# Optimization experiments

Hardware: AMD Instinct MI355X
Metric: run time of the kernel (lower is better)

## Reference

```python
import jax, jax.numpy as jnp
import numpy as np

TWO_PI = 6.283185307179586


def setup_inputs() -> dict:
    key = jax.random.key(0)
    k1, k2, k3, k4, k5, k6 = jax.random.split(key, 6)
    B, T, D = 2, 8192, 1024
    x = jax.random.normal(k1, (B, T, D), dtype=jnp.float32)
    # nn.Linear weights are [out, in]; init with small scale like torch default
    s = 1.0 / np.sqrt(D)
    Wk = jax.random.uniform(k2, (D, D), jnp.float32, -s, s)
    Wv = jax.random.uniform(k3, (D, D), jnp.float32, -s, s)
    Wo = jax.random.uniform(k4, (D, D), jnp.float32, -s, s)
    # random phasor frequencies in [0, 2*pi)
    freqs = jax.random.uniform(k5, (D,), jnp.float32, 0.0, TWO_PI)
    return {"x": x, "Wk": Wk, "Wv": Wv, "Wo": Wo, "freqs": freqs}


def reference(x, Wk, Wv, Wo, freqs):
    B, T, C = x.shape
    # k projection is computed in the original forward but never used downstream
    k_real = x @ Wk.T  # [B,T,D] (dead value, kept for fidelity)
    v_real = x @ Wv.T  # [B,T,D]
    v = v_real.astype(jnp.complex64)
    # rotors: per-position unit phasors exp(i * t * freqs), shape [T, D]
    t = jnp.arange(T, dtype=jnp.float32)
    rotors = jnp.exp(1j * (t[:, None] * freqs[None, :])).astype(jnp.complex64)
    # bind each value with its rotor and accumulate causally (O(N) memory trace)
    memory_trace = jnp.cumsum(v * rotors[None, :, :], axis=1)  # [B,T,D] complex64
    # retrieve by unbinding with the conjugate rotor; take the real component
    retrieved = jnp.real(memory_trace * jnp.conj(rotors)[None, :, :])  # [B,T,D]
    return retrieved @ Wo.T
```

## Files before the change

### kernel.cpp

```cpp
#include <hip/hip_runtime.h>
#include <hip/hip_bf16.h>


#define B_  2
#define T_  8192
#define D_  1024
#define BT_ 16384
#define CS_ 32
#define NCHUNK_ 256

typedef __attribute__((ext_vector_type(4))) float f32x4;
typedef __attribute__((ext_vector_type(8))) short bf16x8;
typedef __attribute__((ext_vector_type(8))) unsigned short ushort8;

static __device__ inline unsigned short f2bf(float f) {
    union { float f; unsigned int u; } a;
    a.f = f;
    unsigned int u = a.u;
    return (unsigned short)((u + 0x7FFFu + ((u >> 16) & 1u)) >> 16);
}
static __device__ inline float bf2f(unsigned short h) {
    union { unsigned int u; float f; } a;
    a.u = ((unsigned int)h) << 16;
    return a.f;
}

__global__ __launch_bounds__(256) void cast_all(const float* __restrict__ x,
                                                const float* __restrict__ Wv,
                                                const float* __restrict__ Wo,
                                                unsigned short* __restrict__ xb,
                                                unsigned short* __restrict__ wvb,
                                                unsigned short* __restrict__ wob) {
    const int nx = BT_ * D_ / 8;
    const int nw = D_ * D_ / 8;
    int i = blockIdx.x * 256 + threadIdx.x;
    const float4* src;
    unsigned short* dst;
    int j;
    if (i < nx)            { src = (const float4*)x;  dst = xb;  j = i; }
    else if (i < nx + nw)  { src = (const float4*)Wv; dst = wvb; j = i - nx; }
    else                   { src = (const float4*)Wo; dst = wob; j = i - nx - nw; }
    float4 a = src[j * 2];
    float4 b = src[j * 2 + 1];
    ushort8 o;
    o[0] = f2bf(a.x); o[1] = f2bf(a.y); o[2] = f2bf(a.z); o[3] = f2bf(a.w);
    o[4] = f2bf(b.x); o[5] = f2bf(b.y); o[6] = f2bf(b.z); o[7] = f2bf(b.w);
    *(ushort8*)&dst[(size_t)j * 8] = o;
}

template <bool BF16OUT, bool FUSE_SUMS>
__global__ __launch_bounds__(512, 2) void gemm_bt(const short* __restrict__ A,
                                                  const short* __restrict__ Bm,
                                                  void* __restrict__ Cout,
                                                  const float* __restrict__ freqs,
                                                  float* __restrict__ csum,
                                                  int M, int N, int K) {
    __shared__ short lds[65536];
    const int tid = threadIdx.x;
    const int lane = tid & 63;
    const int wave = tid >> 6;
    const int wm = wave >> 2, wn = wave & 3;

    const int nb = N >> 8;
    const int id = blockIdx.x;
    const int xcd = id & 7;
    const int slot = id >> 3;
    const int bn = (slot % nb) * 256;
    const int bm = (xcd * ((M >> 8) >> 3) + slot / nb) * 256;

    const int srow = lane >> 3;
    const int sg = lane & 7;
    const size_t cstep = (size_t)64 * K;
    const short* gA = A + (size_t)(bm + wave * 8 + srow) * K + ((sg ^ srow) * 8);
    const short* gB = Bm + (size_t)(bn + wave * 8 + srow) * K + ((sg ^ srow) * 8);

    auto stage1 = [&](int kt, int g) {
        const int c = g & 3;
        const short* src = ((g & 4) ? gB : gA) + c * cstep + kt * 64;
        short* dst = &lds[(kt & 1) * 32768 + ((g & 4) ? 16384 : 0) + c * 4096 + wave * 512];
        __builtin_amdgcn_global_load_lds(
            (const __attribute__((address_space(1))) void*)src,
            (__attribute__((address_space(3))) void*)dst, 16, 0, 0);
    };

    const int l15 = lane & 15;
    const int c4r = lane >> 4;
    const int swz0 = ((c4r) ^ (lane & 7)) * 8;
    const int swz1 = ((4 + c4r) ^ (lane & 7)) * 8;
    const int abase = (wm * 128 + l15) * 64;
    const int bbase = 16384 + (wn * 64 + l15) * 64;

    f32x4 acc[8][4] = {};

    stage1(0, 0); stage1(0, 1); stage1(0, 2); stage1(0, 3);
    stage1(0, 4); stage1(0, 5); stage1(0, 6); stage1(0, 7);
    stage1(1, 0); stage1(1, 2);
    stage1(1, 4); stage1(1, 5); stage1(1, 6); stage1(1, 7);
    asm volatile("s_waitcnt vmcnt(6)" ::: "memory");
    __builtin_amdgcn_sched_barrier(0);
    __builtin_amdgcn_s_barrier();

    const int NT = K >> 6;
#pragma unroll 1
    for (int t = 0; t < NT; ++t) {
        const int sb = (t & 1) * 32768;
        const bool pf = (t + 2 < NT);
        bf16x8 av[4][2], b01[2][2], b23[2][2];

#pragma unroll
        for (int ii = 0; ii < 4; ++ii) {
            av[ii][0] = *(const bf16x8*)&lds[sb + abase + ii * 1024 + swz0];
            av[ii][1] = *(const bf16x8*)&lds[sb + abase + ii * 1024 + swz1];
        }
#pragma unroll
        for (int j = 0; j < 2; ++j) {
            b01[j][0] = *(const bf16x8*)&lds[sb + bbase + j * 1024 + swz0];
            b01[j][1] = *(const bf16x8*)&lds[sb + bbase + j * 1024 + swz1];
        }
        if (t + 1 < NT) { stage1(t + 1, 1); stage1(t + 1, 3); }
        __builtin_amdgcn_s_barrier();
        asm volatile("s_waitcnt lgkmcnt(0)" ::: "memory");
        __builtin_amdgcn_sched_barrier(0);
        __builtin_amdgcn_s_setprio(1);
#pragma unroll
        for (int ks = 0; ks < 2; ++ks)
#pragma unroll
            for (int ii = 0; ii < 4; ++ii)
#pragma unroll
                for (int j = 0; j < 2; ++j)
                    acc[ii][j] = __builtin_amdgcn_mfma_f32_16x16x32_bf16(
                        av[ii][ks], b01[j][ks], acc[ii][j], 0, 0, 0);
        __builtin_amdgcn_s_setprio(0);
        __builtin_amdgcn_s_barrier();

#pragma unroll
        for (int j = 0; j < 2; ++j) {
            b23[j][0] = *(const bf16x8*)&lds[sb + bbase + (2 + j) * 1024 + swz0];
            b23[j][1] = *(const bf16x8*)&lds[sb + bbase + (2 + j) * 1024 + swz1];
        }
        if (pf) { stage1(t + 2, 0); stage1(t + 2, 2); }
        __builtin_amdgcn_s_barrier();
        asm volatile("s_waitcnt lgkmcnt(0)" ::: "memory");
        __builtin_amdgcn_sched_barrier(0);
        __builtin_amdgcn_s_setprio(1);
#pragma unroll
        for (int ks = 0; ks < 2; ++ks)
#pragma unroll
            for (int ii = 0; ii < 4; ++ii)
#pragma unroll
                for (int j = 0; j < 2; ++j)
                    acc[ii][2 + j] = __builtin_amdgcn_mfma_f32_16x16x32_bf16(
                        av[ii][ks], b23[j][ks], acc[ii][2 + j], 0, 0, 0);
        __builtin_amdgcn_s_setprio(0);
        __builtin_amdgcn_s_barrier();

#pragma unroll
        for (int ii = 0; ii < 4; ++ii) {
            av[ii][0] = *(const bf16x8*)&lds[sb + abase + (4 + ii) * 1024 + swz0];
            av[ii][1] = *(const bf16x8*)&lds[sb + abase + (4 + ii) * 1024 + swz1];
        }
        if (pf) { stage1(t + 2, 4); stage1(t + 2, 5); }
        asm volatile("s_waitcnt vmcnt(12)" ::: "memory");
        __builtin_amdgcn_s_barrier();
        asm volatile("s_waitcnt lgkmcnt(0)" ::: "memory");
        __builtin_amdgcn_sched_barrier(0);
        __builtin_amdgcn_s_setprio(1);
#pragma unroll
        for (int ks = 0; ks < 2; ++ks)
#pragma unroll
            for (int ii = 0; ii < 4; ++ii)
#pragma unroll
                for (int j = 0; j < 2; ++j)
                    acc[4 + ii][2 + j] = __builtin_amdgcn_mfma_f32_16x16x32_bf16(
                        av[ii][ks], b23[j][ks], acc[4 + ii][2 + j], 0, 0, 0);
        __builtin_amdgcn_s_setprio(0);
        __builtin_amdgcn_s_barrier();

        if (pf) { stage1(t + 2, 6); stage1(t + 2, 7); }
        if (pf) asm volatile("s_waitcnt vmcnt(8)" ::: "memory");
        else    asm volatile("s_waitcnt vmcnt(0)" ::: "memory");
        __builtin_amdgcn_sched_barrier(0);
        __builtin_amdgcn_s_barrier();
        __builtin_amdgcn_s_setprio(1);
#pragma unroll
        for (int ks = 0; ks < 2; ++ks)
#pragma unroll
            for (int ii = 0; ii < 4; ++ii)
#pragma unroll
                for (int j = 0; j < 2; ++j)
                    acc[4 + ii][j] = __builtin_amdgcn_mfma_f32_16x16x32_bf16(
                        av[ii][ks], b01[j][ks], acc[4 + ii][j], 0, 0, 0);
        __builtin_amdgcn_s_setprio(0);
        __builtin_amdgcn_s_barrier();
    }

    const int row0 = c4r * 4;
#pragma unroll
    for (int i = 0; i < 8; ++i) {
#pragma unroll
        for (int j = 0; j < 4; ++j) {
            const int col = bn + wn * 64 + j * 16 + (lane & 15);
#pragma unroll
            for (int r = 0; r < 4; ++r) {
                const size_t row = (size_t)bm + wm * 128 + i * 16 + row0 + r;
                if constexpr (BF16OUT)
                    ((unsigned short*)Cout)[row * N + col] = f2bf(acc[i][j][r]);
                else
                    ((float*)Cout)[row * N + col] = acc[i][j][r];
            }
        }
    }

    if constexpr (FUSE_SUMS) {
        const int b = bm >> 13;
        const int trow = bm & 8191;
#pragma unroll
        for (int ig2 = 0; ig2 < 4; ++ig2) {
            const int chunk = (trow >> 5) + wm * 4 + ig2;
            const int t0 = trow + wm * 128 + ig2 * 32 + c4r * 4;
#pragma unroll
            for (int j = 0; j < 4; ++j) {
                const int d = bn + wn * 64 + j * 16 + (lane & 15);
                const float f = freqs[d];
                float ss, cc2;
                sincosf((float)t0 * f, &ss, &cc2);
                float s1, c1;
                sincosf(f, &s1, &c1);
                float c2 = c1 * c1 - s1 * s1, s2 = 2.f * c1 * s1;
                float c4 = c2 * c2 - s2 * s2, s4 = 2.f * c2 * s2;
                float c8 = c4 * c4 - s4 * s4, s8 = 2.f * c4 * s4;
                float c12 = c8 * c4 - s8 * s4, s12 = s8 * c4 + c8 * s4;
                float c13 = c12 * c1 - s12 * s1, s13 = s12 * c1 + c12 * s1;
                float ar = 0.f, ai = 0.f;
                float cr = cc2, sr2 = ss;
#pragma unroll
                for (int f2 = 0; f2 < 2; ++f2) {
                    const int i = ig2 * 2 + f2;
#pragma unroll
                    for (int r = 0; r < 4; ++r) {
                        const float w = acc[i][j][r];
                        ar = fmaf(w, cr, ar); ai = fmaf(w, sr2, ai);
                        const float ec = (r < 3) ? c1 : c13;
                        const float es = (r < 3) ? s1 : s13;
                        const float nc = cr * ec - sr2 * es;
                        const float ns = sr2 * ec + cr * es;
                        cr = nc; sr2 = ns;
                    }
                }
                ar += __shfl_xor(ar, 16); ai += __shfl_xor(ai, 16);
                ar += __shfl_xor(ar, 32); ai += __shfl_xor(ai, 32);
                if (c4r == 0)
                    *(float2*)(csum + (((size_t)b * NCHUNK_ + chunk) * D_ + d) * 2) =
                        make_float2(ar, ai);
            }
        }
    }
}

__global__ __launch_bounds__(512) void scan_pass2(float* __restrict__ csum) {
    const int wid = (blockIdx.x * 512 + threadIdx.x) >> 6;
    const int lane = threadIdx.x & 63;
    const int b = wid / D_;
    const int d = wid % D_;
    float2* cs = (float2*)csum;
    const size_t base = (size_t)b * NCHUNK_ * D_ + d;

    float2 s[4];
#pragma unroll
    for (int k = 0; k < 4; ++k)
        s[k] = cs[base + (size_t)(lane * 4 + k) * D_];
    float lr = s[0].x + s[1].x + s[2].x + s[3].x;
    float li = s[0].y + s[1].y + s[2].y + s[3].y;

    float ir = lr, ii = li;
#pragma unroll
    for (int off = 1; off < 64; off <<= 1) {
        float tr = __shfl_up(ir, off);
        float ti = __shfl_up(ii, off);
        if (lane >= off) { ir += tr; ii += ti; }
    }
    float er = ir - lr, ei = ii - li;
#pragma unroll
    for (int k = 0; k < 4; ++k) {
        const float rr = s[k].x, rim = s[k].y;
        cs[base + (size_t)(lane * 4 + k) * D_] = make_float2(er, ei);
        er += rr; ei += rim;
    }
}

__global__ __launch_bounds__(256) void scan_pass3(const unsigned short* __restrict__ v,
                                                  const float* __restrict__ freqs,
                                                  const float* __restrict__ csum,
                                                  unsigned short* __restrict__ ret) {
    const int chunk = blockIdx.x;
    const int d0 = blockIdx.y * 512 + threadIdx.x * 2;
    const int b = blockIdx.z;

    float fr[2], s[2], c[2], sf[2], cf[2], ar[2], ai[2];
    {
        float2 f2 = *(const float2*)(freqs + d0);
        fr[0] = f2.x; fr[1] = f2.y;
    }
    const float t0f = (float)(chunk * CS_);
#pragma unroll
    for (int k = 0; k < 2; ++k) {
        sincosf(t0f * fr[k], &s[k], &c[k]);
        sincosf(fr[k], &sf[k], &cf[k]);
    }
    {
        const float4 o = *(const float4*)(csum + (((size_t)b * NCHUNK_ + chunk) * D_ + d0) * 2);
        ar[0] = o.x; ai[0] = o.y; ar[1] = o.z; ai[1] = o.w;
    }
    const unsigned int* vp = (const unsigned int*)(v + ((size_t)b * T_ + chunk * CS_) * D_ + d0);
    unsigned int* rp = (unsigned int*)(ret + ((size_t)b * T_ + chunk * CS_) * D_ + d0);
    for (int tb = 0; tb < CS_; tb += 8) {
        unsigned int w[8];
#pragma unroll
        for (int u = 0; u < 8; ++u) w[u] = vp[(size_t)(tb + u) * (D_ / 2)];
#pragma unroll
        for (int u = 0; u < 8; ++u) {
            float wv[2], o[2];
            wv[0] = bf2f((unsigned short)w[u]);
            wv[1] = bf2f((unsigned short)(w[u] >> 16));
#pragma unroll
            for (int k = 0; k < 2; ++k) {
                ar[k] = fmaf(wv[k], c[k], ar[k]);
                ai[k] = fmaf(wv[k], s[k], ai[k]);
                o[k] = ar[k] * c[k] + ai[k] * s[k];
                float nc = c[k] * cf[k] - s[k] * sf[k];
                float ns = s[k] * cf[k] + c[k] * sf[k];
                c[k] = nc; s[k] = ns;
            }
            rp[(size_t)(tb + u) * (D_ / 2)] =
                (unsigned int)f2bf(o[0]) | ((unsigned int)f2bf(o[1]) << 16);
        }
    }
}

extern "C" void kernel_launch(void* const* d_in, const int* in_sizes, int n_in,
                              void* d_out, int out_size, void* d_ws, size_t ws_size,
                              hipStream_t stream) {
    const float* x     = (const float*)d_in[0];
    const float* Wv    = (const float*)d_in[2];
    const float* Wo    = (const float*)d_in[3];
    const float* freqs = (const float*)d_in[4];
    float* out = (float*)d_out;

    char* ws = (char*)d_ws;
    unsigned short* x_bf  = (unsigned short*)ws;
    unsigned short* Wv_bf = (unsigned short*)(ws + 33554432);
    unsigned short* Wo_bf = (unsigned short*)(ws + 35651584);
    float*          csum  = (float*)(ws + 37748736);
    unsigned short* ret  = (unsigned short*)ws;
    unsigned short* v_bf = (unsigned short*)d_out;

    cast_all<<<(BT_ * D_ / 8 + 2 * D_ * D_ / 8) / 256, 256, 0, stream>>>(
        x, Wv, Wo, x_bf, Wv_bf, Wo_bf);

    gemm_bt<true, true><<<(BT_ / 256) * (D_ / 256), 512, 0, stream>>>(
        (const short*)x_bf, (const short*)Wv_bf, (void*)v_bf, freqs, csum, BT_, D_, D_);

    scan_pass2<<<(B_ * D_ * 64) / 512, 512, 0, stream>>>(csum);
    dim3 p3grid(NCHUNK_, D_ / 512, B_);
    scan_pass3<<<p3grid, 256, 0, stream>>>(v_bf, freqs, csum, ret);

    gemm_bt<false, false><<<(BT_ / 256) * (D_ / 256), 512, 0, stream>>>(
        (const short*)ret, (const short*)Wo_bf, (void*)out, nullptr, nullptr, BT_, D_, D_);
}
```

Baseline: 234.9 us.

## Fuse fp32-to-bf16 cast of x into first GEMM's A-tile load path

```diff
diff --git a/kernel.cpp b/kernel.cpp
--- a/kernel.cpp
+++ b/kernel.cpp
@@ -25,21 +25,17 @@
     return a.f;
 }
 
-__global__ __launch_bounds__(256) void cast_all(const float* __restrict__ x,
-                                                const float* __restrict__ Wv,
-                                                const float* __restrict__ Wo,
-                                                unsigned short* __restrict__ xb,
-                                                unsigned short* __restrict__ wvb,
-                                                unsigned short* __restrict__ wob) {
-    const int nx = BT_ * D_ / 8;
+__global__ __launch_bounds__(256) void cast_w(const float* __restrict__ Wv,
+                                              const float* __restrict__ Wo,
+                                              unsigned short* __restrict__ wvb,
+                                              unsigned short* __restrict__ wob) {
     const int nw = D_ * D_ / 8;
     int i = blockIdx.x * 256 + threadIdx.x;
     const float4* src;
     unsigned short* dst;
     int j;
-    if (i < nx)            { src = (const float4*)x;  dst = xb;  j = i; }
-    else if (i < nx + nw)  { src = (const float4*)Wv; dst = wvb; j = i - nx; }
-    else                   { src = (const float4*)Wo; dst = wob; j = i - nx - nw; }
+    if (i < nw) { src = (const float4*)Wv; dst = wvb; j = i; }
+    else        { src = (const float4*)Wo; dst = wob; j = i - nw; }
     float4 a = src[j * 2];
     float4 b = src[j * 2 + 1];
     ushort8 o;
@@ -48,8 +44,8 @@
     *(ushort8*)&dst[(size_t)j * 8] = o;
 }
 
-template <bool BF16OUT, bool FUSE_SUMS>
-__global__ __launch_bounds__(512, 2) void gemm_bt(const short* __restrict__ A,
+template <bool CAST_A, bool BF16OUT, bool FUSE_SUMS>
+__global__ __launch_bounds__(512, 2) void gemm_bt(const void* __restrict__ Av,
                                                   const short* __restrict__ Bm,
                                                   void* __restrict__ Cout,
                                                   const float* __restrict__ freqs,
@@ -71,8 +67,11 @@
     const int srow = lane >> 3;
     const int sg = lane & 7;
     const size_t cstep = (size_t)64 * K;
-    const short* gA = A + (size_t)(bm + wave * 8 + srow) * K + ((sg ^ srow) * 8);
+    const short* A16 = (const short*)Av;
+    const float* A32 = (const float*)Av;
+    const short* gA = A16 + (size_t)(bm + wave * 8 + srow) * K + ((sg ^ srow) * 8);
     const short* gB = Bm + (size_t)(bn + wave * 8 + srow) * K + ((sg ^ srow) * 8);
+    const float* gAf = A32 + (size_t)(bm + wave * 8 + srow) * K + sg * 8;
 
     auto stage1 = [&](int kt, int g) {
         const int c = g & 3;
@@ -83,6 +82,27 @@
             (__attribute__((address_space(3))) void*)dst, 16, 0, 0);
     };
 
+    auto issueA = [&](float4 (&ar)[4][2], int kt) {
+#pragma unroll
+        for (int g = 0; g < 4; ++g) {
+            const float4* p = (const float4*)(gAf + (size_t)g * cstep + kt * 64);
+            ar[g][0] = p[0];
+            ar[g][1] = p[1];
+        }
+    };
+    const int awbase = (wave * 8 + srow) * 64 + (sg ^ srow) * 8;
+    auto writeA = [&](float4 (&ar)[4][2], int kt) {
+#pragma unroll
+        for (int g = 0; g < 4; ++g) {
+            bf16x8 v;
+            v[0] = (short)f2bf(ar[g][0].x); v[1] = (short)f2bf(ar[g][0].y);
+            v[2] = (short)f2bf(ar[g][0].z); v[3] = (short)f2bf(ar[g][0].w);
+            v[4] = (short)f2bf(ar[g][1].x); v[5] = (short)f2bf(ar[g][1].y);
+            v[6] = (short)f2bf(ar[g][1].z); v[7] = (short)f2bf(ar[g][1].w);
+            *(bf16x8*)&lds[(kt & 1) * 32768 + g * 4096 + awbase] = v;
+        }
+    };
+
     const int l15 = lane & 15;
     const int c4r = lane >> 4;
     const int swz0 = ((c4r) ^ (lane & 7)) * 8;
@@ -91,12 +111,24 @@
     const int bbase = 16384 + (wn * 64 + l15) * 64;
 
     f32x4 acc[8][4] = {};
-
-    stage1(0, 0); stage1(0, 1); stage1(0, 2); stage1(0, 3);
-    stage1(0, 4); stage1(0, 5); stage1(0, 6); stage1(0, 7);
-    stage1(1, 0); stage1(1, 2);
-    stage1(1, 4); stage1(1, 5); stage1(1, 6); stage1(1, 7);
-    asm volatile("s_waitcnt vmcnt(6)" ::: "memory");
+    float4 aA[4][2], aB[4][2];
+
+    if constexpr (CAST_A) {
+        issueA(aA, 0);
+        stage1(0, 4); stage1(0, 5); stage1(0, 6); stage1(0, 7);
+        issueA(aB, 1);
+        asm volatile("s_waitcnt vmcnt(12)" ::: "memory");
+        writeA(aA, 0);
+        stage1(1, 4); stage1(1, 5); stage1(1, 6); stage1(1, 7);
+        asm volatile("s_waitcnt vmcnt(12)" ::: "memory");
+        asm volatile("s_waitcnt lgkmcnt(0)" ::: "memory");
+    } else {
+        stage1(0, 0); stage1(0, 1); stage1(0, 2); stage1(0, 3);
+        stage1(0, 4); stage1(0, 5); stage1(0, 6); stage1(0, 7);
+        stage1(1, 0); stage1(1, 2);
+        stage1(1, 4); stage1(1, 5); stage1(1, 6); stage1(1, 7);
+        asm volatile("s_waitcnt vmcnt(6)" ::: "memory");
+    }
     __builtin_amdgcn_sched_barrier(0);
     __builtin_amdgcn_s_barrier();
 
@@ -117,7 +149,11 @@
             b01[j][0] = *(const bf16x8*)&lds[sb + bbase + j * 1024 + swz0];
             b01[j][1] = *(const bf16x8*)&lds[sb + bbase + j * 1024 + swz1];
         }
-        if (t + 1 < NT) { stage1(t + 1, 1); stage1(t + 1, 3); }
+        if constexpr (CAST_A) {
+            if (pf) { if ((t & 1) == 0) issueA(aA, t + 2); else issueA(aB, t + 2); }
+        } else {
+            if (t + 1 < NT) { stage1(t + 1, 1); stage1(t + 1, 3); }
+        }
         __builtin_amdgcn_s_barrier();
         asm volatile("s_waitcnt lgkmcnt(0)" ::: "memory");
         __builtin_amdgcn_sched_barrier(0);
@@ -138,7 +174,9 @@
             b23[j][0] = *(const bf16x8*)&lds[sb + bbase + (2 + j) * 1024 + swz0];
             b23[j][1] = *(const bf16x8*)&lds[sb + bbase + (2 + j) * 1024 + swz1];
         }
-        if (pf) { stage1(t + 2, 0); stage1(t + 2, 2); }
+        if constexpr (!CAST_A) {
+            if (pf) { stage1(t + 2, 0); stage1(t + 2, 2); }
+        }
         __builtin_amdgcn_s_barrier();
         asm volatile("s_waitcnt lgkmcnt(0)" ::: "memory");
         __builtin_amdgcn_sched_barrier(0);
@@ -159,8 +197,14 @@
             av[ii][0] = *(const bf16x8*)&lds[sb + abase + (4 + ii) * 1024 + swz0];
             av[ii][1] = *(const bf16x8*)&lds[sb + abase + (4 + ii) * 1024 + swz1];
         }
+        if constexpr (CAST_A) {
+            if (t + 1 < NT) {
+                if (pf) asm volatile("s_waitcnt vmcnt(12)" ::: "memory");
+                else    asm volatile("s_waitcnt vmcnt(4)" ::: "memory");
+                if ((t & 1) == 1) writeA(aA, t + 1); else writeA(aB, t + 1);
+            }
+        }
         if (pf) { stage1(t + 2, 4); stage1(t + 2, 5); }
-        asm volatile("s_waitcnt vmcnt(12)" ::: "memory");
         __builtin_amdgcn_s_barrier();
         asm volatile("s_waitcnt lgkmcnt(0)" ::: "memory");
         __builtin_amdgcn_sched_barrier(0);
@@ -177,8 +221,13 @@
         __builtin_amdgcn_s_barrier();
 
         if (pf) { stage1(t + 2, 6); stage1(t + 2, 7); }
-        if (pf) asm volatile("s_waitcnt vmcnt(8)" ::: "memory");
-        else    asm volatile("s_waitcnt vmcnt(0)" ::: "memory");
+        if constexpr (CAST_A) {
+            if (pf) asm volatile("s_waitcnt vmcnt(12)" ::: "memory");
+            else    asm volatile("s_waitcnt vmcnt(0)" ::: "memory");
+        } else {
+            if (pf) asm volatile("s_waitcnt vmcnt(8)" ::: "memory");
+            else    asm volatile("s_waitcnt vmcnt(0)" ::: "memory");
+        }
         __builtin_amdgcn_sched_barrier(0);
         __builtin_amdgcn_s_barrier();
         __builtin_amdgcn_s_setprio(1);
@@ -347,23 +396,21 @@
     float* out = (float*)d_out;
 
     char* ws = (char*)d_ws;
-    unsigned short* x_bf  = (unsigned short*)ws;
+    unsigned short* ret   = (unsigned short*)ws;
     unsigned short* Wv_bf = (unsigned short*)(ws + 33554432);
     unsigned short* Wo_bf = (unsigned short*)(ws + 35651584);
     float*          csum  = (float*)(ws + 37748736);
-    unsigned short* ret  = (unsigned short*)ws;
     unsigned short* v_bf = (unsigned short*)d_out;
 
-    cast_all<<<(BT_ * D_ / 8 + 2 * D_ * D_ / 8) / 256, 256, 0, stream>>>(
-        x, Wv, Wo, x_bf, Wv_bf, Wo_bf);
-
-    gemm_bt<true, true><<<(BT_ / 256) * (D_ / 256), 512, 0, stream>>>(
-        (const short*)x_bf, (const short*)Wv_bf, (void*)v_bf, freqs, csum, BT_, D_, D_);
+    cast_w<<<(2 * D_ * D_ / 8) / 256, 256, 0, stream>>>(Wv, Wo, Wv_bf, Wo_bf);
+
+    gemm_bt<true, true, true><<<(BT_ / 256) * (D_ / 256), 512, 0, stream>>>(
+        (const void*)x, (const short*)Wv_bf, (void*)v_bf, freqs, csum, BT_, D_, D_);
 
     scan_pass2<<<(B_ * D_ * 64) / 512, 512, 0, stream>>>(csum);
     dim3 p3grid(NCHUNK_, D_ / 512, B_);
     scan_pass3<<<p3grid, 256, 0, stream>>>(v_bf, freqs, csum, ret);
 
-    gemm_bt<false, false><<<(BT_ / 256) * (D_ / 256), 512, 0, stream>>>(
-        (const short*)ret, (const short*)Wo_bf, (void*)out, nullptr, nullptr, BT_, D_, D_);
-}
+    gemm_bt<false, false, false><<<(BT_ / 256) * (D_ / 256), 512, 0, stream>>>(
+        (const void*)ret, (const short*)Wo_bf, (void*)out, nullptr, nullptr, BT_, D_, D_);
+}
```

Result: slower. 400.0 us (+70.3%).
